# Performance work log

Hardware: AMD Instinct MI355X
Metric: run time of the kernel (lower is better)

Reference implementation:

```python
import jax, jax.numpy as jnp
import numpy as np

RADIUS = 0.2
NSAMPLE = 32
USE_XYZ = True

B, N, NPOINT, C = 4, 16384, 2048, 64


def setup_inputs() -> dict:
    key = jax.random.key(0)
    k1, k2, k3 = jax.random.split(key, 3)
    xyz = jax.random.uniform(k1, (B, N, 3), dtype=jnp.float32)
    new_xyz = jax.random.uniform(k2, (B, NPOINT, 3), dtype=jnp.float32)
    features = jax.random.normal(k3, (B, C, N), dtype=jnp.float32)
    return {"xyz": xyz, "new_xyz": new_xyz, "features": features}


def _ball_query(radius, nsample, xyz, new_xyz):
    # xyz: (B,N,3), new_xyz: (B,S,3) -> idx: (B,S,nsample) int32
    d2 = jnp.sum((new_xyz[:, :, None, :] - xyz[:, None, :, :]) ** 2, axis=-1)  # (B,S,N)
    mask = d2 < radius * radius
    # stable sort puts in-ball indices first, preserving original order
    order = jnp.argsort(~mask, axis=-1, stable=True)  # (B,S,N)
    idx = order[..., :nsample]  # first nsample in-ball indices (or fillers)
    count = jnp.sum(mask, axis=-1, dtype=jnp.int32)  # (B,S)
    slot_valid = jnp.arange(nsample, dtype=jnp.int32)[None, None, :] < count[..., None]
    # pad with the first valid index (index 0 if the ball is empty),
    # matching the reference CUDA ball_query behavior
    idx = jnp.where(slot_valid, idx, idx[..., :1])
    return idx.astype(jnp.int32)


def _group(features, idx):
    # features: (B,C,N), idx: (B,S,K) -> (B,C,S,K)
    return jnp.take_along_axis(features[:, :, None, :], idx[:, None, :, :], axis=3)


def reference(xyz, new_xyz, features):
    idx = _ball_query(RADIUS, NSAMPLE, xyz, new_xyz)  # (B,S,K)
    xyz_t = jnp.transpose(xyz, (0, 2, 1))  # (B,3,N)
    grouped_xyz = _group(xyz_t, idx)  # (B,3,S,K)
    grouped_xyz = grouped_xyz - jnp.transpose(new_xyz, (0, 2, 1))[..., None]
    grouped_features = _group(features, idx)  # (B,C,S,K)
    if USE_XYZ:
        new_features = jnp.concatenate([grouped_xyz, grouped_features], axis=1)
    else:
        new_features = grouped_features
    return new_features  # (B, 3+C, S, K)
```

## Files before the change

kernel.cpp:

```cpp
#include <hip/hip_runtime.h>


namespace {
constexpr int kN   = 16384;
constexpr int kNP  = 2048;
constexpr int kC   = 64;
constexpr int kNS  = 32;
constexpr int kOC  = 3 + kC;
constexpr int kWin = 256;
}

__device__ __forceinline__ float d2_rn(float nx, float ny, float nz,
                                       float px, float py, float pz) {
    const float dx = __fsub_rn(nx, px);
    const float dy = __fsub_rn(ny, py);
    const float dz = __fsub_rn(nz, pz);
    return __fadd_rn(__fadd_rn(__fmul_rn(dx, dx), __fmul_rn(dy, dy)),
                     __fmul_rn(dz, dz));
}

__global__ __launch_bounds__(256) void tr_kernel(
    const float* __restrict__ feat, float* __restrict__ tf)
{
    __shared__ float tile[64][65];
    const int b  = blockIdx.x >> 8;
    const int n0 = (blockIdx.x & 255) << 6;
    const float* fb = feat + (size_t)b * kC * kN;
    float* ob       = tf   + (size_t)b * kN * kC;
    const int t  = threadIdx.x;
    const int q  = t >> 6;
    const int nn = t & 63;
    #pragma unroll
    for (int p = 0; p < 16; ++p) {
        const int c = p * 4 + q;
        tile[c][nn] = __builtin_nontemporal_load(&fb[(size_t)c * kN + n0 + nn]);
    }
    __syncthreads();
    const int cc = t & 63;
    #pragma unroll
    for (int p = 0; p < 16; ++p) {
        const int n = p * 4 + q;
        ob[(size_t)(n0 + n) * kC + cc] = tile[cc][n];
    }
}

__global__ __launch_bounds__(128) void qg_fused(
    const float* __restrict__ xyz,
    const float* __restrict__ new_xyz,
    const float* __restrict__ tf,
    float* __restrict__ out)
{
    __shared__ int sIdx[2][kNS];
    const int t = threadIdx.x;
    const int w = t >> 6;
    const int l = t & 63;

    const int qid = (blockIdx.x << 1) | w;
    const int b   = qid >> 11;
    const int j   = qid & 2047;

    const float* __restrict__ xb = xyz + (size_t)b * kN * 3;
    const float4* __restrict__ xv = reinterpret_cast<const float4*>(xb);
    const float* nxp = new_xyz + ((size_t)b * kNP + j) * 3;
    const float nx = nxp[0], ny = nxp[1], nz = nxp[2];
    const float R2 = 0.04f;

    int count = 0;
    float4 A0, A1, A2, B0, B1, B2;
    {
        const int o = 3 * l;
        B0 = xv[o]; B1 = xv[o + 1]; B2 = xv[o + 2];
    }
    for (int base = 0; base < kN; base += kWin) {
        A0 = B0; A1 = B1; A2 = B2;
        if (base + kWin < kN) {
            const int o = ((base + kWin) >> 2) * 3 + 3 * l;
            B0 = xv[o]; B1 = xv[o + 1]; B2 = xv[o + 2];
        }
        const float d0  = d2_rn(nx, ny, nz, A0.x, A0.y, A0.z);
        const float d1  = d2_rn(nx, ny, nz, A0.w, A1.x, A1.y);
        const float d2v = d2_rn(nx, ny, nz, A1.z, A1.w, A2.x);
        const float d3  = d2_rn(nx, ny, nz, A2.y, A2.z, A2.w);
        const unsigned long long b0 = __ballot(d0  < R2);
        const unsigned long long b1 = __ballot(d1  < R2);
        const unsigned long long b2 = __ballot(d2v < R2);
        const unsigned long long b3 = __ballot(d3  < R2);

        const unsigned long long m = (1ull << l) - 1ull;
        int slot = count + (int)(__popcll(b0 & m) + __popcll(b1 & m) +
                                 __popcll(b2 & m) + __popcll(b3 & m));
        const int i0 = base + 4 * l;
        if (d0  < R2) { if (slot < kNS) sIdx[w][slot] = i0 + 0; ++slot; }
        if (d1  < R2) { if (slot < kNS) sIdx[w][slot] = i0 + 1; ++slot; }
        if (d2v < R2) { if (slot < kNS) sIdx[w][slot] = i0 + 2; ++slot; }
        if (d3  < R2) { if (slot < kNS) sIdx[w][slot] = i0 + 3; ++slot; }

        count += (int)(__popcll(b0) + __popcll(b1) +
                       __popcll(b2) + __popcll(b3));
        if (count >= kNS) break;
    }
    __builtin_amdgcn_wave_barrier();

    if (count == 0) {
        if (l < kNS) sIdx[w][l] = 0;
    } else if (count < kNS) {
        const int first = sIdx[w][0];
        __builtin_amdgcn_wave_barrier();
        if (l >= count && l < kNS) sIdx[w][l] = first;
    }
    __builtin_amdgcn_wave_barrier();

    const int s = l & 31;
    const int h = l >> 5;
    const int id = sIdx[w][s];

    const size_t cs = (size_t)kNP * kNS;
    float* ob = out + ((size_t)b * kOC * kNP + j) * kNS + s;

    if (h == 0) {
        const float g0 = xb[(size_t)id * 3 + 0] - nx;
        const float g1 = xb[(size_t)id * 3 + 1] - ny;
        const float g2 = xb[(size_t)id * 3 + 2] - nz;
        __builtin_nontemporal_store(g0, &ob[0 * cs]);
        __builtin_nontemporal_store(g1, &ob[1 * cs]);
        __builtin_nontemporal_store(g2, &ob[2 * cs]);
    }

    const float* row = tf + ((size_t)b * kN + id) * kC;
    float* obf = ob + 3 * cs;
    #pragma unroll
    for (int it = 0; it < 8; ++it) {
        const int chunk = it * 2 + h;
        const float4 v = *reinterpret_cast<const float4*>(row + chunk * 4);
        const size_t c0 = (size_t)chunk * 4;
        __builtin_nontemporal_store(v.x, &obf[(c0 + 0) * cs]);
        __builtin_nontemporal_store(v.y, &obf[(c0 + 1) * cs]);
        __builtin_nontemporal_store(v.z, &obf[(c0 + 2) * cs]);
        __builtin_nontemporal_store(v.w, &obf[(c0 + 3) * cs]);
    }
}

__global__ __launch_bounds__(256) void qg_direct(
    const float* __restrict__ xyz, const float* __restrict__ new_xyz,
    const float* __restrict__ feat, float* __restrict__ out)
{
    __shared__ int sIdx[4][kNS];
    const int wave = threadIdx.x >> 6;
    const int lane = threadIdx.x & 63;
    const int bid  = blockIdx.x;
    const int xcd  = bid & 7;
    const int b    = xcd >> 1;
    const int jblk = ((xcd & 1) << 8) | (bid >> 3);
    const int j    = (jblk << 2) | wave;

    const float* __restrict__ xb = xyz + (size_t)b * kN * 3;
    const float* nxp = new_xyz + ((size_t)b * kNP + j) * 3;
    const float nx = nxp[0], ny = nxp[1], nz = nxp[2];
    const float R2 = 0.04f;

    int count = 0;
    for (int base = 0; base < kN; base += 64) {
        const int i = base + lane;
        const float d2 = d2_rn(nx, ny, nz, xb[(size_t)i * 3 + 0],
                               xb[(size_t)i * 3 + 1], xb[(size_t)i * 3 + 2]);
        const bool in = d2 < R2;
        const unsigned long long bal = __ballot(in);
        const int pre  = (int)__popcll(bal & ((1ull << lane) - 1ull));
        const int slot = count + pre;
        if (in && slot < kNS) sIdx[wave][slot] = i;
        count += (int)__popcll(bal);
        if (count >= kNS) break;
    }
    __builtin_amdgcn_wave_barrier();
    if (count == 0) {
        if (lane < kNS) sIdx[wave][lane] = 0;
    } else if (count < kNS) {
        const int first = sIdx[wave][0];
        __builtin_amdgcn_wave_barrier();
        if (lane >= count && lane < kNS) sIdx[wave][lane] = first;
    }
    __builtin_amdgcn_wave_barrier();

    const int s    = lane & 31;
    const int half = lane >> 5;
    const int id   = sIdx[wave][s];
    const float g0 = xb[(size_t)id * 3 + 0] - nx;
    const float g1 = xb[(size_t)id * 3 + 1] - ny;
    const float g2 = xb[(size_t)id * 3 + 2] - nz;
    const size_t cs = (size_t)kNP * kNS;
    float* ob = out + (((size_t)b * kOC) * kNP + j) * kNS + s;
    const float* fb = feat + ((size_t)b * kC) * kN + id;
    #pragma unroll
    for (int cb = 0; cb < kOC; cb += 2) {
        const int c = cb + half;
        if (c < kOC) {
            float v;
            if (c < 3) v = (c == 0) ? g0 : ((c == 1) ? g1 : g2);
            else       v = fb[(size_t)(c - 3) * kN];
            ob[(size_t)c * cs] = v;
        }
    }
}

extern "C" void kernel_launch(void* const* d_in, const int* in_sizes, int n_in,
                              void* d_out, int out_size, void* d_ws, size_t ws_size,
                              hipStream_t stream) {
    const float* xyz     = (const float*)d_in[0];
    const float* new_xyz = (const float*)d_in[1];
    const float* feat    = (const float*)d_in[2];
    float* out           = (float*)d_out;

    const size_t tf_bytes = (size_t)4 * kN * kC * sizeof(float);
    if (ws_size >= tf_bytes) {
        float* tf = (float*)d_ws;
        tr_kernel<<<dim3(1024), dim3(256), 0, stream>>>(feat, tf);
        qg_fused <<<dim3(4096), dim3(128), 0, stream>>>(xyz, new_xyz, tf, out);
    } else {
        qg_direct<<<dim3(2048), dim3(256), 0, stream>>>(xyz, new_xyz, feat, out);
    }
}
```

Before: 112.3 us.

## Split into ball-query index kernel and LDS-cached per-channel gather kernel

Drops the feature transpose kernel. The ball query now writes its indices to a workspace buffer. A new gather kernel stages one full feature channel (64 KB) in shared memory and writes output rows with coalesced vector stores by reading indices from that buffer. The ball query also widens its scan window so each lane tests 16 points per step, and uses 4 waves per block. This trades the transpose round-trip and the strided per-channel scalar stores for an extra index buffer pass. The 64 KB of LDS per block limits occupancy.

```diff
diff --git a/kernel.cpp b/kernel.cpp
--- a/kernel.cpp
+++ b/kernel.cpp
@@ -7,8 +7,10 @@
 constexpr int kC   = 64;
 constexpr int kNS  = 32;
 constexpr int kOC  = 3 + kC;
-constexpr int kWin = 256;
-}
+constexpr int kWin = 1024;
+}
+
+typedef float vf4 __attribute__((ext_vector_type(4)));
 
 __device__ __forceinline__ float d2_rn(float nx, float ny, float nz,
                                        float px, float py, float pz) {
@@ -19,43 +21,18 @@
                      __fmul_rn(dz, dz));
 }
 
-__global__ __launch_bounds__(256) void tr_kernel(
-    const float* __restrict__ feat, float* __restrict__ tf)
-{
-    __shared__ float tile[64][65];
-    const int b  = blockIdx.x >> 8;
-    const int n0 = (blockIdx.x & 255) << 6;
-    const float* fb = feat + (size_t)b * kC * kN;
-    float* ob       = tf   + (size_t)b * kN * kC;
-    const int t  = threadIdx.x;
-    const int q  = t >> 6;
-    const int nn = t & 63;
-    #pragma unroll
-    for (int p = 0; p < 16; ++p) {
-        const int c = p * 4 + q;
-        tile[c][nn] = __builtin_nontemporal_load(&fb[(size_t)c * kN + n0 + nn]);
-    }
-    __syncthreads();
-    const int cc = t & 63;
-    #pragma unroll
-    for (int p = 0; p < 16; ++p) {
-        const int n = p * 4 + q;
-        ob[(size_t)(n0 + n) * kC + cc] = tile[cc][n];
-    }
-}
-
-__global__ __launch_bounds__(128) void qg_fused(
+__global__ __launch_bounds__(256) void bq_kernel(
     const float* __restrict__ xyz,
     const float* __restrict__ new_xyz,
-    const float* __restrict__ tf,
+    int*   __restrict__ idxbuf,
     float* __restrict__ out)
 {
-    __shared__ int sIdx[2][kNS];
+    __shared__ int sIdx[4][kNS];
     const int t = threadIdx.x;
     const int w = t >> 6;
     const int l = t & 63;
 
-    const int qid = (blockIdx.x << 1) | w;
+    const int qid = (blockIdx.x << 2) | w;
     const int b   = qid >> 11;
     const int j   = qid & 2047;
 
@@ -66,37 +43,41 @@
     const float R2 = 0.04f;
 
     int count = 0;
-    float4 A0, A1, A2, B0, B1, B2;
+    float4 buf[12];
     {
-        const int o = 3 * l;
-        B0 = xv[o]; B1 = xv[o + 1]; B2 = xv[o + 2];
+        const int f0 = 12 * l;
+        #pragma unroll
+        for (int k = 0; k < 12; ++k) buf[k] = xv[f0 + k];
     }
     for (int base = 0; base < kN; base += kWin) {
-        A0 = B0; A1 = B1; A2 = B2;
+        const float* p = reinterpret_cast<const float*>(buf);
+        unsigned int hm = 0;
+        #pragma unroll
+        for (int k = 0; k < 16; ++k) {
+            const float d = d2_rn(nx, ny, nz, p[3*k], p[3*k+1], p[3*k+2]);
+            hm |= (d < R2) ? (1u << k) : 0u;
+        }
         if (base + kWin < kN) {
-            const int o = ((base + kWin) >> 2) * 3 + 3 * l;
-            B0 = xv[o]; B1 = xv[o + 1]; B2 = xv[o + 2];
-        }
-        const float d0  = d2_rn(nx, ny, nz, A0.x, A0.y, A0.z);
-        const float d1  = d2_rn(nx, ny, nz, A0.w, A1.x, A1.y);
-        const float d2v = d2_rn(nx, ny, nz, A1.z, A1.w, A2.x);
-        const float d3  = d2_rn(nx, ny, nz, A2.y, A2.z, A2.w);
-        const unsigned long long b0 = __ballot(d0  < R2);
-        const unsigned long long b1 = __ballot(d1  < R2);
-        const unsigned long long b2 = __ballot(d2v < R2);
-        const unsigned long long b3 = __ballot(d3  < R2);
-
+            const int f0 = 3 * ((base + kWin) >> 2) + 12 * l;
+            #pragma unroll
+            for (int k = 0; k < 12; ++k) buf[k] = xv[f0 + k];
+        }
         const unsigned long long m = (1ull << l) - 1ull;
-        int slot = count + (int)(__popcll(b0 & m) + __popcll(b1 & m) +
-                                 __popcll(b2 & m) + __popcll(b3 & m));
-        const int i0 = base + 4 * l;
-        if (d0  < R2) { if (slot < kNS) sIdx[w][slot] = i0 + 0; ++slot; }
-        if (d1  < R2) { if (slot < kNS) sIdx[w][slot] = i0 + 1; ++slot; }
-        if (d2v < R2) { if (slot < kNS) sIdx[w][slot] = i0 + 2; ++slot; }
-        if (d3  < R2) { if (slot < kNS) sIdx[w][slot] = i0 + 3; ++slot; }
-
-        count += (int)(__popcll(b0) + __popcll(b1) +
-                       __popcll(b2) + __popcll(b3));
+        int pre = 0, wtot = 0;
+        unsigned long long bal[16];
+        #pragma unroll
+        for (int k = 0; k < 16; ++k) {
+            bal[k] = __ballot((hm >> k) & 1u);
+            pre  += (int)__popcll(bal[k] & m);
+            wtot += (int)__popcll(bal[k]);
+        }
+        int slot = count + pre;
+        const int i0 = base + 16 * l;
+        #pragma unroll
+        for (int k = 0; k < 16; ++k) {
+            if ((hm >> k) & 1u) { if (slot < kNS) sIdx[w][slot] = i0 + k; ++slot; }
+        }
+        count += wtot;
         if (count >= kNS) break;
     }
     __builtin_amdgcn_wave_barrier();
@@ -110,33 +91,59 @@
     }
     __builtin_amdgcn_wave_barrier();
 
+    if (l < kNS) idxbuf[(size_t)qid * kNS + l] = sIdx[w][l];
+
     const int s = l & 31;
     const int h = l >> 5;
-    const int id = sIdx[w][s];
-
-    const size_t cs = (size_t)kNP * kNS;
-    float* ob = out + ((size_t)b * kOC * kNP + j) * kNS + s;
-
     if (h == 0) {
-        const float g0 = xb[(size_t)id * 3 + 0] - nx;
-        const float g1 = xb[(size_t)id * 3 + 1] - ny;
-        const float g2 = xb[(size_t)id * 3 + 2] - nz;
-        __builtin_nontemporal_store(g0, &ob[0 * cs]);
-        __builtin_nontemporal_store(g1, &ob[1 * cs]);
-        __builtin_nontemporal_store(g2, &ob[2 * cs]);
-    }
-
-    const float* row = tf + ((size_t)b * kN + id) * kC;
-    float* obf = ob + 3 * cs;
+        const int id = sIdx[w][s];
+        const size_t cs = (size_t)kNP * kNS;
+        float* ob = out + ((size_t)b * kOC * kNP + j) * kNS + s;
+        __builtin_nontemporal_store(xb[(size_t)id * 3 + 0] - nx, &ob[0 * cs]);
+        __builtin_nontemporal_store(xb[(size_t)id * 3 + 1] - ny, &ob[1 * cs]);
+        __builtin_nontemporal_store(xb[(size_t)id * 3 + 2] - nz, &ob[2 * cs]);
+    }
+}
+
+__global__ __launch_bounds__(256) void cg_kernel(
+    const float* __restrict__ feat,
+    const int*   __restrict__ idxbuf,
+    float* __restrict__ out)
+{
+    __shared__ float col[kN];
+    const int t = threadIdx.x;
+
+    const int bid = blockIdx.x;
+    const int h   = (bid >> 3) & 1;
+    const int u   = (bid & 7) | ((bid >> 4) << 3);
+    const int b   = u >> 6;
+    const int c   = u & 63;
+
+    const float4* fv = reinterpret_cast<const float4*>(
+        feat + ((size_t)b * kC + c) * kN);
+    float4* cv = reinterpret_cast<float4*>(col);
     #pragma unroll
-    for (int it = 0; it < 8; ++it) {
-        const int chunk = it * 2 + h;
-        const float4 v = *reinterpret_cast<const float4*>(row + chunk * 4);
-        const size_t c0 = (size_t)chunk * 4;
-        __builtin_nontemporal_store(v.x, &obf[(c0 + 0) * cs]);
-        __builtin_nontemporal_store(v.y, &obf[(c0 + 1) * cs]);
-        __builtin_nontemporal_store(v.z, &obf[(c0 + 2) * cs]);
-        __builtin_nontemporal_store(v.w, &obf[(c0 + 3) * cs]);
+    for (int k = 0; k < 16; ++k) cv[t + k * 256] = fv[t + k * 256];
+    __syncthreads();
+
+    const int sq = t >> 3;
+    const int s8 = t & 7;
+    const int jbase = h << 10;
+    float* ob = out + (((size_t)b * kOC + 3 + c) * kNP) * kNS;
+    const int4* iv = reinterpret_cast<const int4*>(idxbuf);
+
+    #pragma unroll 4
+    for (int p = 0; p < 32; ++p) {
+        const int j   = jbase + p * 32 + sq;
+        const int qid = (b << 11) | j;
+        const int4 i4 = iv[(size_t)qid * 8 + s8];
+        vf4 v;
+        v.x = col[i4.x];
+        v.y = col[i4.y];
+        v.z = col[i4.z];
+        v.w = col[i4.w];
+        __builtin_nontemporal_store(
+            v, reinterpret_cast<vf4*>(&ob[(size_t)j * kNS + (s8 << 2)]));
     }
 }
 
@@ -210,11 +217,12 @@
     const float* feat    = (const float*)d_in[2];
     float* out           = (float*)d_out;
 
-    const size_t tf_bytes = (size_t)4 * kN * kC * sizeof(float);
-    if (ws_size >= tf_bytes) {
-        float* tf = (float*)d_ws;
-        tr_kernel<<<dim3(1024), dim3(256), 0, stream>>>(feat, tf);
-        qg_fused <<<dim3(4096), dim3(128), 0, stream>>>(xyz, new_xyz, tf, out);
+    const size_t idx_bytes = (size_t)4 * kNP * kNS * sizeof(int);
+    if (ws_size >= idx_bytes) {
+        int* idxbuf = (int*)d_ws;
+        bq_kernel<<<dim3(2048), dim3(256), 0, stream>>>(
+            xyz, new_xyz, idxbuf, out);
+        cg_kernel<<<dim3(512), dim3(256), 0, stream>>>(feat, idxbuf, out);
     } else {
         qg_direct<<<dim3(2048), dim3(256), 0, stream>>>(xyz, new_xyz, feat, out);
     }
```

Measured after the change: 116.9 us. 1.04x slower.
